# Optimization experiments

Measured on AMD Instinct MI355X. Metric: run time of the kernel, lower is better.

## Reference

```python
import jax, jax.numpy as jnp
import numpy as np
import math

B, SQ, SK = 8, 1024, 1024
DQ = DK = DV = 1024
H = 16
EPS = 1e-5


def _layer_norm(x, g, b):
    mu = jnp.mean(x, axis=-1, keepdims=True)
    var = jnp.mean(jnp.square(x - mu), axis=-1, keepdims=True)
    return (x - mu) * jax.lax.rsqrt(var + EPS) * g + b


def setup_inputs() -> dict:
    key = jax.random.key(0)
    ks = jax.random.split(key, 8)
    s_q = 1.0 / math.sqrt(DQ)
    s_v = 1.0 / math.sqrt(DV)
    return {
        "Q": jax.random.normal(ks[0], (B, SQ, DQ), dtype=jnp.float32),
        "K": jax.random.normal(ks[1], (B, SK, DK), dtype=jnp.float32),
        "Wq": jax.random.normal(ks[2], (DQ, DV), dtype=jnp.float32) * s_q,
        "bq": jnp.zeros((DV,), dtype=jnp.float32),
        "Wk": jax.random.normal(ks[3], (DK, DV), dtype=jnp.float32) * s_q,
        "bk": jnp.zeros((DV,), dtype=jnp.float32),
        "Wv": jax.random.normal(ks[4], (DK, DV), dtype=jnp.float32) * s_q,
        "bv": jnp.zeros((DV,), dtype=jnp.float32),
        "Wo": jax.random.normal(ks[5], (DV, DV), dtype=jnp.float32) * s_v,
        "bo": jnp.zeros((DV,), dtype=jnp.float32),
        "g0": jnp.ones((DV,), dtype=jnp.float32),
        "b0": jnp.zeros((DV,), dtype=jnp.float32),
        "g1": jnp.ones((DV,), dtype=jnp.float32),
        "b1": jnp.zeros((DV,), dtype=jnp.float32),
    }


def reference(Q, K, Wq, bq, Wk, bk, Wv, bv, Wo, bo, g0, b0, g1, b1):
    dh = DV // H
    q = Q @ Wq + bq                      # [B,SQ,DV]
    k = K @ Wk + bk                      # [B,SK,DV]
    v = K @ Wv + bv                      # [B,SK,DV]
    # split/cat over heads == reshape to [B,S,H,dh]
    qh = q.reshape(B, SQ, H, dh)
    kh = k.reshape(B, SK, H, dh)
    vh = v.reshape(B, SK, H, dh)
    # NOTE: original scales by sqrt(dim_V), not sqrt(head_dim)
    scores = jnp.einsum("bqhd,bkhd->bhqk", qh, kh) / math.sqrt(DV)
    A = jax.nn.softmax(scores, axis=-1)  # [B,H,SQ,SK]
    attn = jnp.einsum("bhqk,bkhd->bqhd", A, vh)
    out = q + attn.reshape(B, SQ, DV)    # residual with projected Q
    out = _layer_norm(out, g0, b0)
    out = out + jax.nn.relu(out @ Wo + bo)
    out = _layer_norm(out, g1, b1)
    return out
```

## Files before the change

kernel.cpp:

```cpp
#include <hip/hip_runtime.h>
#include <hip/hip_bf16.h>
#include <stdint.h>

#define NB 8
#define NSQ 1024
#define NSK 1024
#define ND 1024
#define NH 16
#define NDH 64
#define NM (NB * NSQ)
#define LOG2E 1.4426950408889634f

typedef __bf16 bf16;
typedef __bf16 bf16x8 __attribute__((ext_vector_type(8)));
typedef float f32x4 __attribute__((ext_vector_type(4)));
typedef float f32x16 __attribute__((ext_vector_type(16)));
typedef unsigned int uint32;

__device__ __forceinline__ void async_load16(const void* g, void* l) {
  __builtin_amdgcn_global_load_lds(
      (__attribute__((address_space(1))) void*)g,
      (__attribute__((address_space(3))) void*)l, 16, 0, 0);
}

__device__ __forceinline__ void permswap(uint32& x, uint32& y) {
#if __has_builtin(__builtin_amdgcn_permlane32_swap)
  auto r = __builtin_amdgcn_permlane32_swap(x, y, false, false);
  x = r[0]; y = r[1];
#else
  asm volatile("v_permlane32_swap_b32 %0, %1" : "+v"(x), "+v"(y));
#endif
}

__global__ __launch_bounds__(256) void cvt2_f32_bf16(const float* __restrict__ A,
                                                     const float* __restrict__ B,
                                                     bf16* __restrict__ Oa,
                                                     bf16* __restrict__ Ob) {
  const float* in = blockIdx.y ? B : A;
  bf16* out = blockIdx.y ? Ob : Oa;
  int i = blockIdx.x * 256 + threadIdx.x;
  float4 v = *(const float4*)(in + (size_t)i * 4);
  union { uint64_t u; bf16 h[4]; } o;
  o.h[0] = (bf16)v.x; o.h[1] = (bf16)v.y; o.h[2] = (bf16)v.z; o.h[3] = (bf16)v.w;
  *(uint64_t*)(out + (size_t)i * 4) = o.u;
}

__global__ __launch_bounds__(256) void transpose_cvt4(
    const float* __restrict__ W0, const float* __restrict__ W1,
    const float* __restrict__ W2, const float* __restrict__ W3,
    bf16* __restrict__ O0, bf16* __restrict__ O1,
    bf16* __restrict__ O2, bf16* __restrict__ O3) {
  const float* W; bf16* Wt;
  switch (blockIdx.z) {
    case 0: W = W0; Wt = O0; break;
    case 1: W = W1; Wt = O1; break;
    case 2: W = W2; Wt = O2; break;
    default: W = W3; Wt = O3; break;
  }
  __shared__ float t[64][65];
  const int bc = blockIdx.x * 64;
  const int br = blockIdx.y * 64;
  const int tid = threadIdx.x;
  for (int c = tid; c < 1024; c += 256) {
    int r = c >> 4, off = (c & 15) * 4;
    float4 v = *(const float4*)&W[(size_t)(br + r) * 1024 + bc + off];
    t[r][off] = v.x; t[r][off + 1] = v.y; t[r][off + 2] = v.z; t[r][off + 3] = v.w;
  }
  __syncthreads();
  for (int c = tid; c < 512; c += 256) {
    int cc = c >> 3, rr = (c & 7) * 8;
    union { uint4 u; bf16 h[8]; } o;
#pragma unroll
    for (int i = 0; i < 8; ++i) o.h[i] = (bf16)t[rr + i][cc];
    *(uint4*)&Wt[(size_t)(bc + cc) * 1024 + br + rr] = o.u;
  }
}

__global__ __launch_bounds__(256) void transpose_v(const bf16* __restrict__ vsrc,
                                                   bf16* __restrict__ vT) {
  const int st = blockIdx.x * 64;
  const int bh = blockIdx.y;
  const int b = bh >> 4, h = bh & 15;
  __shared__ __align__(16) bf16 t[64][72];
  const int tid = threadIdx.x;
  for (int c = tid; c < 512; c += 256) {
    int s = c >> 3, off = (c & 7) * 8;
    *(uint4*)&t[s][off] =
        *(const uint4*)&vsrc[(size_t)(b * NSK + st + s) * 2048 + 1024 + h * NDH + off];
  }
  __syncthreads();
  for (int c = tid; c < 512; c += 256) {
    int d = c >> 3, s0 = (c & 7) * 8;
    union { uint4 u; bf16 h[8]; } o;
#pragma unroll
    for (int i = 0; i < 8; ++i) o.h[i] = t[s0 + i][d];
    *(uint4*)&vT[((size_t)(bh * NDH + d)) * NSK + st + s0] = o.u;
  }
}

template <int BM, int MODE, int NXC>
__global__ __launch_bounds__(256, 2) void gemm3b(
    const bf16* __restrict__ A, const bf16* __restrict__ Bt,
    const float* __restrict__ bias, const float* __restrict__ bias2,
    bf16* __restrict__ Cb, const bf16* __restrict__ Resb, float scale, int N) {
  constexpr int NT = 32;
  constexpr int AR = BM / 64;
  constexpr int MR = BM / 32;
  __shared__ __align__(16) bf16 Asl[3][BM * 32];
  __shared__ __align__(16) bf16 Bsl[3][128 * 32];

  const int tid = threadIdx.x;
  const int flat = blockIdx.x;
  const int xi = (flat & 7) * 64 + (flat >> 3);
  const int bcol = (xi & (NXC - 1)) * 128;
  const int brow = (xi / NXC) * BM;

  const int w = tid >> 6, lane = tid & 63;
  const int wm = w >> 1, wn = w & 1;
  const int lr = lane & 15, l4 = lane >> 4;
  const int rgrp = l4 * 4;
  const int gph = (l4 ^ ((lr >> 1) & 3)) * 8;

  const int srow = tid >> 2;
  const int gsrc = (tid & 3) ^ ((tid >> 3) & 3);
  const bf16* Ag = A + (size_t)(brow + srow) * 1024 + gsrc * 8;
  const bf16* Bg = Bt + (size_t)(bcol + srow) * 1024 + gsrc * 8;
  const int ldo = srow * 32 + (tid & 3) * 8;

  auto stage = [&](int d, int kt) {
#pragma unroll
    for (int r = 0; r < AR; ++r)
      async_load16(Ag + (size_t)r * (64 * 1024) + kt * 32, &Asl[d][r * 2048 + ldo]);
#pragma unroll
    for (int r = 0; r < 2; ++r)
      async_load16(Bg + (size_t)r * (64 * 1024) + kt * 32, &Bsl[d][r * 2048 + ldo]);
  };
  auto wait_tile = [&]() {
    if constexpr (BM == 256) asm volatile("s_waitcnt vmcnt(6)" ::: "memory");
    else                     asm volatile("s_waitcnt vmcnt(4)" ::: "memory");
  };

  f32x4 acc[MR][4] = {};

  stage(0, 0);
  stage(1, 1);
  wait_tile();
  __builtin_amdgcn_s_barrier();

  int cur = 0, st2 = 2;
  for (int t = 0; t < NT; ++t) {
    bf16x8 af[MR], bfr[4];
#pragma unroll
    for (int i = 0; i < MR; ++i)
      af[i] = *(const bf16x8*)&Asl[cur][(wm * (BM / 2) + i * 16 + lr) * 32 + gph];
#pragma unroll
    for (int n = 0; n < 4; ++n)
      bfr[n] = *(const bf16x8*)&Bsl[cur][(wn * 64 + n * 16 + lr) * 32 + gph];
    if (t + 2 < NT) stage(st2, t + 2);
    __builtin_amdgcn_s_setprio(1);
#pragma unroll
    for (int i = 0; i < MR; ++i)
#pragma unroll
      for (int n = 0; n < 4; ++n)
        acc[i][n] = __builtin_amdgcn_mfma_f32_16x16x32_bf16(af[i], bfr[n], acc[i][n], 0, 0, 0);
    __builtin_amdgcn_s_setprio(0);
    if (t + 2 < NT)      wait_tile();
    else if (t + 1 < NT) asm volatile("s_waitcnt vmcnt(0)" ::: "memory");
    asm volatile("s_waitcnt lgkmcnt(0)" ::: "memory");
    __builtin_amdgcn_s_barrier();
    cur = (cur == 2) ? 0 : cur + 1;
    st2 = (st2 == 2) ? 0 : st2 + 1;
  }

#pragma unroll
  for (int m = 0; m < MR; ++m) {
#pragma unroll
    for (int n = 0; n < 4; ++n) {
      const int col = bcol + wn * 64 + n * 16 + lr;
      float bv, sc;
      if (MODE == 2) {
        const bool isV = (bcol >= 1024);
        bv = isV ? bias2[col - 1024] : bias[col];
        sc = isV ? 1.0f : LOG2E;
      } else {
        bv = bias[col];
        sc = scale;
      }
#pragma unroll
      for (int r = 0; r < 4; ++r) {
        const int row = brow + wm * (BM / 2) + m * 16 + rgrp + r;
        float v = acc[m][n][r] + bv;
        if (MODE == 1) {
          float res = (float)Resb[(size_t)row * N + col];
          Cb[(size_t)row * N + col] = (bf16)(res + (v > 0.f ? v : 0.f));
        } else {
          Cb[(size_t)row * N + col] = (bf16)(v * sc);
        }
      }
    }
  }
}

__global__ __launch_bounds__(512, 4) void attn_kernel(
    const bf16* __restrict__ qb, const bf16* __restrict__ kvb,
    const bf16* __restrict__ vT, bf16* __restrict__ attnout) {
  const int bh = blockIdx.y;
  const int b = bh >> 4, h = bh & 15;
  const int tid = threadIdx.x, w = tid >> 6, lane = tid & 63;
  const int l31 = lane & 31;
  const int l1 = lane >> 5;
  const int q0w = blockIdx.x * 256 + w * 32;

  __shared__ __align__(16) bf16 Kl[2][64 * 64];
  __shared__ __align__(16) bf16 Vl[2][64 * 64];

  const int srow = tid >> 3;
  const int sgran = tid & 7;
  const int gsw = sgran ^ (srow & 7);
  const int ldst = srow * 64 + sgran * 8;
  const int rg = l31 & 7;

  const bf16* kbase = kvb + (size_t)(b * NSK) * 2048 + h * NDH;
  const bf16* vbase = vT + (size_t)(bh * NDH) * NSK;

  bf16x8 qf[4];
#pragma unroll
  for (int kd = 0; kd < 4; ++kd)
    qf[kd] = *(const bf16x8*)&qb[(size_t)(b * NSQ + q0w + l31) * ND +
                                 h * NDH + kd * 16 + l1 * 8];

  f32x16 oacc0 = {}, oacc1 = {}, lacc = {};
  bf16x8 ones;
#pragma unroll
  for (int i = 0; i < 8; ++i) ones[i] = (bf16)1.0f;

  auto stage = [&](int bi, int kt) {
    async_load16(kbase + (size_t)(kt + srow) * 2048 + gsw * 8, &Kl[bi][ldst]);
    async_load16(vbase + (size_t)srow * NSK + kt + gsw * 8, &Vl[bi][ldst]);
  };

  stage(0, 0);

  for (int t = 0; t < 16; ++t) {
    const int bi = t & 1;
    asm volatile("s_waitcnt vmcnt(0)" ::: "memory");
    __syncthreads();
    if (t < 15) stage(bi ^ 1, (t + 1) * 64);

    uint32 W[2][4][2];
#pragma unroll
    for (int n = 0; n < 2; ++n) {
      f32x16 s = {};
      __builtin_amdgcn_s_setprio(1);
#pragma unroll
      for (int kd = 0; kd < 4; ++kd) {
        bf16x8 kf = *(const bf16x8*)&Kl[bi][(n * 32 + l31) * 64 + (((kd * 2 + l1) ^ rg) * 8)];
        s = __builtin_amdgcn_mfma_f32_32x32x16_bf16(kf, qf[kd], s, 0, 0, 0);
      }
      __builtin_amdgcn_s_setprio(0);
#pragma unroll
      for (int r2 = 0; r2 < 4; ++r2)
#pragma unroll
        for (int p = 0; p < 2; ++p) {
          float elo = __builtin_amdgcn_exp2f(s[r2 * 4 + 2 * p]);
          float ehi = __builtin_amdgcn_exp2f(s[r2 * 4 + 2 * p + 1]);
          uint32 wd;
          asm("v_cvt_pk_bf16_f32 %0, %1, %2" : "=v"(wd) : "v"(elo), "v"(ehi));
          W[n][r2][p] = wd;
        }
    }
    __builtin_amdgcn_s_setprio(1);
#pragma unroll
    for (int kc = 0; kc < 4; ++kc) {
      uint32 x0 = W[kc >> 1][(kc & 1) * 2][0], y0 = W[kc >> 1][(kc & 1) * 2 + 1][0];
      uint32 x1 = W[kc >> 1][(kc & 1) * 2][1], y1 = W[kc >> 1][(kc & 1) * 2 + 1][1];
      permswap(x0, y0);
      permswap(x1, y1);
      union { uint32 u[4]; bf16x8 v; } cvt;
      cvt.u[0] = x0; cvt.u[1] = x1; cvt.u[2] = y0; cvt.u[3] = y1;
      bf16x8 pa = cvt.v;
      bf16x8 vf0 = *(const bf16x8*)&Vl[bi][(l31) * 64 + (((kc * 2 + l1) ^ rg) * 8)];
      bf16x8 vf1 = *(const bf16x8*)&Vl[bi][(32 + l31) * 64 + (((kc * 2 + l1) ^ rg) * 8)];
      oacc0 = __builtin_amdgcn_mfma_f32_32x32x16_bf16(pa, vf0, oacc0, 0, 0, 0);
      oacc1 = __builtin_amdgcn_mfma_f32_32x32x16_bf16(pa, vf1, oacc1, 0, 0, 0);
      lacc = __builtin_amdgcn_mfma_f32_32x32x16_bf16(pa, ones, lacc, 0, 0, 0);
    }
    __builtin_amdgcn_s_setprio(0);
  }

  float inv[16];
#pragma unroll
  for (int r = 0; r < 16; ++r) inv[r] = 1.0f / lacc[r];
#pragma unroll
  for (int r = 0; r < 16; ++r) {
    const int row = q0w + (r & 3) + 8 * (r >> 2) + 4 * l1;
    attnout[(size_t)(b * NSQ + row) * ND + h * NDH + l31] = (bf16)(oacc0[r] * inv[r]);
    attnout[(size_t)(b * NSQ + row) * ND + h * NDH + 32 + l31] = (bf16)(oacc1[r] * inv[r]);
  }
}

template <bool RES, bool OUTF>
__global__ __launch_bounds__(256) void ln_kernel(
    const bf16* __restrict__ x, const bf16* __restrict__ rq, float rscale,
    const float* __restrict__ g, const float* __restrict__ be,
    bf16* __restrict__ yb, float* __restrict__ yf) {
  __shared__ float sm[4];
  const int row = blockIdx.x, tid = threadIdx.x;
  const size_t base = (size_t)row * ND + tid * 4;
  union { uint2 u; bf16 h[4]; } xv;
  xv.u = *(const uint2*)(x + base);
  float v0 = (float)xv.h[0], v1 = (float)xv.h[1], v2 = (float)xv.h[2], v3 = (float)xv.h[3];
  if (RES) {
    union { uint2 u; bf16 h[4]; } q;
    q.u = *(const uint2*)(rq + base);
    v0 += rscale * (float)q.h[0]; v1 += rscale * (float)q.h[1];
    v2 += rscale * (float)q.h[2]; v3 += rscale * (float)q.h[3];
  }
  float s = v0 + v1 + v2 + v3;
#pragma unroll
  for (int off = 32; off > 0; off >>= 1) s += __shfl_down(s, off, 64);
  if ((tid & 63) == 0) sm[tid >> 6] = s;
  __syncthreads();
  const float mean = (sm[0] + sm[1] + sm[2] + sm[3]) * (1.0f / ND);
  __syncthreads();
  const float d0 = v0 - mean, d1 = v1 - mean, d2 = v2 - mean, d3 = v3 - mean;
  float sq = d0 * d0 + d1 * d1 + d2 * d2 + d3 * d3;
#pragma unroll
  for (int off = 32; off > 0; off >>= 1) sq += __shfl_down(sq, off, 64);
  if ((tid & 63) == 0) sm[tid >> 6] = sq;
  __syncthreads();
  const float var = (sm[0] + sm[1] + sm[2] + sm[3]) * (1.0f / ND);
  const float rs = rsqrtf(var + 1e-5f);
  float4 gv = *(const float4*)(g + tid * 4);
  float4 bv = *(const float4*)(be + tid * 4);
  const float y0 = d0 * rs * gv.x + bv.x;
  const float y1 = d1 * rs * gv.y + bv.y;
  const float y2 = d2 * rs * gv.z + bv.z;
  const float y3 = d3 * rs * gv.w + bv.w;
  if (OUTF) {
    *(float4*)(yf + base) = make_float4(y0, y1, y2, y3);
  } else {
    union { uint2 u; bf16 h[4]; } o;
    o.h[0] = (bf16)y0; o.h[1] = (bf16)y1; o.h[2] = (bf16)y2; o.h[3] = (bf16)y3;
    *(uint2*)(yb + base) = o.u;
  }
}

extern "C" void kernel_launch(void* const* d_in, const int* in_sizes, int n_in,
                              void* d_out, int out_size, void* d_ws, size_t ws_size,
                              hipStream_t stream) {
  const float* Q  = (const float*)d_in[0];
  const float* K  = (const float*)d_in[1];
  const float* Wq = (const float*)d_in[2];
  const float* bq = (const float*)d_in[3];
  const float* Wk = (const float*)d_in[4];
  const float* bk = (const float*)d_in[5];
  const float* Wv = (const float*)d_in[6];
  const float* bv = (const float*)d_in[7];
  const float* Wo = (const float*)d_in[8];
  const float* bo = (const float*)d_in[9];
  const float* g0 = (const float*)d_in[10];
  const float* b0 = (const float*)d_in[11];
  const float* g1 = (const float*)d_in[12];
  const float* b1 = (const float*)d_in[13];
  float* out = (float*)d_out;

  char* ws = (char*)d_ws;
  const size_t MB = 1024 * 1024;
  bf16* Qb    = (bf16*)(ws + 0);
  bf16* Kb    = (bf16*)(ws + 16 * MB);
  bf16* Wqt   = (bf16*)(ws + 32 * MB);
  bf16* Wkvt  = (bf16*)(ws + 34 * MB);
  bf16* Wot   = (bf16*)(ws + 38 * MB);
  bf16* qb    = (bf16*)(ws + 40 * MB);
  bf16* kvb   = (bf16*)(ws + 56 * MB);
  bf16* vT    = (bf16*)(ws + 88 * MB);
  bf16* attnb = (bf16*)(ws + 104 * MB);
  bf16* h0b   = (bf16*)(ws + 56 * MB);
  bf16* out1b = (bf16*)(ws + 0);

  cvt2_f32_bf16<<<dim3(8192, 2), 256, 0, stream>>>(Q, K, Qb, Kb);
  transpose_cvt4<<<dim3(16, 16, 4), 256, 0, stream>>>(
      Wq, Wk, Wv, Wo, Wqt, Wkvt, Wkvt + 1024 * 1024, Wot);
  gemm3b<256, 2, 16><<<512, 256, 0, stream>>>(Kb, Wkvt, bk, bv, kvb, nullptr, 1.0f, 2048);
  gemm3b<128, 0, 8><<<512, 256, 0, stream>>>(Qb, Wqt, bq, nullptr, qb, nullptr, 0.03125f, 1024);
  transpose_v<<<dim3(16, 128), 256, 0, stream>>>(kvb, vT);
  attn_kernel<<<dim3(4, 128), 512, 0, stream>>>(qb, kvb, vT, attnb);
  ln_kernel<true, false><<<8192, 256, 0, stream>>>(attnb, qb, 32.0f, g0, b0, h0b, nullptr);
  gemm3b<128, 1, 8><<<512, 256, 0, stream>>>(h0b, Wot, bo, nullptr, out1b, h0b, 1.0f, 1024);
  ln_kernel<false, true><<<8192, 256, 0, stream>>>(out1b, nullptr, 0.f, g1, b1, nullptr, out);
}
```

Baseline: 180.3 us.

## Use 2-wave 256x128 GEMM tiles and remap attention grid for L2 locality

Replaces the 4-wave GEMM kernel with a 2-wave version in which each wave computes a 128x128 sub-tile (8x8 MFMA accumulators), raising per-wave register reuse of LDS fragments, and shrinks the Q and Wo projection grids to 256 blocks of 256x128. The attention kernel moves to a flat 1D grid with a swizzled block-to-(batch,head,q-tile) mapping so that concurrently running blocks are spread across XCDs and share K/V in cache. Risks include very high VGPR use (256 accumulator floats per lane), lower occupancy, and fewer blocks than CUs for the 256-block GEMMs.

```diff
diff --git a/kernel.cpp b/kernel.cpp
--- a/kernel.cpp
+++ b/kernel.cpp
@@ -98,25 +98,23 @@
   }
 }
 
-template <int BM, int MODE, int NXC>
-__global__ __launch_bounds__(256, 2) void gemm3b(
+template <int MODE, int NXC>
+__global__ __launch_bounds__(128) void gemmW(
     const bf16* __restrict__ A, const bf16* __restrict__ Bt,
     const float* __restrict__ bias, const float* __restrict__ bias2,
     bf16* __restrict__ Cb, const bf16* __restrict__ Resb, float scale, int N) {
   constexpr int NT = 32;
-  constexpr int AR = BM / 64;
-  constexpr int MR = BM / 32;
-  __shared__ __align__(16) bf16 Asl[3][BM * 32];
+  __shared__ __align__(16) bf16 Asl[3][256 * 32];
   __shared__ __align__(16) bf16 Bsl[3][128 * 32];
 
   const int tid = threadIdx.x;
   const int flat = blockIdx.x;
-  const int xi = (flat & 7) * 64 + (flat >> 3);
+  const int nwg = gridDim.x;
+  const int xi = (flat & 7) * (nwg >> 3) + (flat >> 3);
   const int bcol = (xi & (NXC - 1)) * 128;
-  const int brow = (xi / NXC) * BM;
+  const int brow = (xi / NXC) * 256;
 
   const int w = tid >> 6, lane = tid & 63;
-  const int wm = w >> 1, wn = w & 1;
   const int lr = lane & 15, l4 = lane >> 4;
   const int rgrp = l4 * 4;
   const int gph = (l4 ^ ((lr >> 1) & 3)) * 8;
@@ -129,42 +127,38 @@
 
   auto stage = [&](int d, int kt) {
 #pragma unroll
-    for (int r = 0; r < AR; ++r)
-      async_load16(Ag + (size_t)r * (64 * 1024) + kt * 32, &Asl[d][r * 2048 + ldo]);
-#pragma unroll
-    for (int r = 0; r < 2; ++r)
-      async_load16(Bg + (size_t)r * (64 * 1024) + kt * 32, &Bsl[d][r * 2048 + ldo]);
+    for (int r = 0; r < 8; ++r)
+      async_load16(Ag + (size_t)r * (32 * 1024) + kt * 32, &Asl[d][r * 1024 + ldo]);
+#pragma unroll
+    for (int r = 0; r < 4; ++r)
+      async_load16(Bg + (size_t)r * (32 * 1024) + kt * 32, &Bsl[d][r * 1024 + ldo]);
   };
-  auto wait_tile = [&]() {
-    if constexpr (BM == 256) asm volatile("s_waitcnt vmcnt(6)" ::: "memory");
-    else                     asm volatile("s_waitcnt vmcnt(4)" ::: "memory");
-  };
-
-  f32x4 acc[MR][4] = {};
+
+  f32x4 acc[8][8] = {};
 
   stage(0, 0);
   stage(1, 1);
-  wait_tile();
+  asm volatile("s_waitcnt vmcnt(12)" ::: "memory");
   __builtin_amdgcn_s_barrier();
 
   int cur = 0, st2 = 2;
   for (int t = 0; t < NT; ++t) {
-    bf16x8 af[MR], bfr[4];
-#pragma unroll
-    for (int i = 0; i < MR; ++i)
-      af[i] = *(const bf16x8*)&Asl[cur][(wm * (BM / 2) + i * 16 + lr) * 32 + gph];
-#pragma unroll
-    for (int n = 0; n < 4; ++n)
-      bfr[n] = *(const bf16x8*)&Bsl[cur][(wn * 64 + n * 16 + lr) * 32 + gph];
+    bf16x8 af[8], bfr[8];
+#pragma unroll
+    for (int i = 0; i < 8; ++i)
+      af[i] = *(const bf16x8*)&Asl[cur][(w * 128 + i * 16 + lr) * 32 + gph];
+#pragma unroll
+    for (int n = 0; n < 8; ++n)
+      bfr[n] = *(const bf16x8*)&Bsl[cur][(n * 16 + lr) * 32 + gph];
     if (t + 2 < NT) stage(st2, t + 2);
     __builtin_amdgcn_s_setprio(1);
 #pragma unroll
-    for (int i = 0; i < MR; ++i)
-#pragma unroll
-      for (int n = 0; n < 4; ++n)
+    for (int i = 0; i < 8; ++i)
+#pragma unroll
+      for (int n = 0; n < 8; ++n)
         acc[i][n] = __builtin_amdgcn_mfma_f32_16x16x32_bf16(af[i], bfr[n], acc[i][n], 0, 0, 0);
     __builtin_amdgcn_s_setprio(0);
-    if (t + 2 < NT)      wait_tile();
+    if (t + 2 < NT)      asm volatile("s_waitcnt vmcnt(12)" ::: "memory");
     else if (t + 1 < NT) asm volatile("s_waitcnt vmcnt(0)" ::: "memory");
     asm volatile("s_waitcnt lgkmcnt(0)" ::: "memory");
     __builtin_amdgcn_s_barrier();
@@ -173,10 +167,10 @@
   }
 
 #pragma unroll
-  for (int m = 0; m < MR; ++m) {
-#pragma unroll
-    for (int n = 0; n < 4; ++n) {
-      const int col = bcol + wn * 64 + n * 16 + lr;
+  for (int m = 0; m < 8; ++m) {
+#pragma unroll
+    for (int n = 0; n < 8; ++n) {
+      const int col = bcol + n * 16 + lr;
       float bv, sc;
       if (MODE == 2) {
         const bool isV = (bcol >= 1024);
@@ -188,7 +182,7 @@
       }
 #pragma unroll
       for (int r = 0; r < 4; ++r) {
-        const int row = brow + wm * (BM / 2) + m * 16 + rgrp + r;
+        const int row = brow + w * 128 + m * 16 + rgrp + r;
         float v = acc[m][n][r] + bv;
         if (MODE == 1) {
           float res = (float)Resb[(size_t)row * N + col];
@@ -204,12 +198,14 @@
 __global__ __launch_bounds__(512, 4) void attn_kernel(
     const bf16* __restrict__ qb, const bf16* __restrict__ kvb,
     const bf16* __restrict__ vT, bf16* __restrict__ attnout) {
-  const int bh = blockIdx.y;
+  const int bid = blockIdx.x;
+  const int bh = (bid & 7) + 8 * ((bid >> 3) & 15);
+  const int qi = bid >> 7;
   const int b = bh >> 4, h = bh & 15;
   const int tid = threadIdx.x, w = tid >> 6, lane = tid & 63;
   const int l31 = lane & 31;
   const int l1 = lane >> 5;
-  const int q0w = blockIdx.x * 256 + w * 32;
+  const int q0w = qi * 256 + w * 32;
 
   __shared__ __align__(16) bf16 Kl[2][64 * 64];
   __shared__ __align__(16) bf16 Vl[2][64 * 64];
@@ -382,11 +378,11 @@
   cvt2_f32_bf16<<<dim3(8192, 2), 256, 0, stream>>>(Q, K, Qb, Kb);
   transpose_cvt4<<<dim3(16, 16, 4), 256, 0, stream>>>(
       Wq, Wk, Wv, Wo, Wqt, Wkvt, Wkvt + 1024 * 1024, Wot);
-  gemm3b<256, 2, 16><<<512, 256, 0, stream>>>(Kb, Wkvt, bk, bv, kvb, nullptr, 1.0f, 2048);
-  gemm3b<128, 0, 8><<<512, 256, 0, stream>>>(Qb, Wqt, bq, nullptr, qb, nullptr, 0.03125f, 1024);
+  gemmW<2, 16><<<512, 128, 0, stream>>>(Kb, Wkvt, bk, bv, kvb, nullptr, 1.0f, 2048);
+  gemmW<0, 8><<<256, 128, 0, stream>>>(Qb, Wqt, bq, nullptr, qb, nullptr, 0.03125f, 1024);
   transpose_v<<<dim3(16, 128), 256, 0, stream>>>(kvb, vT);
-  attn_kernel<<<dim3(4, 128), 512, 0, stream>>>(qb, kvb, vT, attnb);
+  attn_kernel<<<512, 512, 0, stream>>>(qb, kvb, vT, attnb);
   ln_kernel<true, false><<<8192, 256, 0, stream>>>(attnb, qb, 32.0f, g0, b0, h0b, nullptr);
-  gemm3b<128, 1, 8><<<512, 256, 0, stream>>>(h0b, Wot, bo, nullptr, out1b, h0b, 1.0f, 1024);
+  gemmW<1, 8><<<256, 128, 0, stream>>>(h0b, Wot, bo, nullptr, out1b, h0b, 1.0f, 1024);
   ln_kernel<false, true><<<8192, 256, 0, stream>>>(out1b, nullptr, 0.f, g1, b1, nullptr, out);
 }
```

Result: slower. 196.8 us (+9.1%).

## Fuse fp32-to-bf16 input conversion into projection GEMM A-tile loads

Applied to the files above, without the earlier changes.

Removes the separate Q/K fp32→bf16 conversion kernel. The K/V and Q projection GEMMs now load fp32 A tiles into registers, convert them, and write them to LDS one stage ahead, while B still uses async global-to-LDS loads. This avoids a 64MB read plus 32MB write pass and one launch. In exchange, the GEMM reads twice the A bytes from fp32, holds more registers, and adds VALU conversion and LDS stores inside the main loop. The wait counts were retuned to match.

```diff
diff --git a/kernel.cpp b/kernel.cpp
--- a/kernel.cpp
+++ b/kernel.cpp
@@ -30,19 +30,6 @@
 #else
   asm volatile("v_permlane32_swap_b32 %0, %1" : "+v"(x), "+v"(y));
 #endif
-}
-
-__global__ __launch_bounds__(256) void cvt2_f32_bf16(const float* __restrict__ A,
-                                                     const float* __restrict__ B,
-                                                     bf16* __restrict__ Oa,
-                                                     bf16* __restrict__ Ob) {
-  const float* in = blockIdx.y ? B : A;
-  bf16* out = blockIdx.y ? Ob : Oa;
-  int i = blockIdx.x * 256 + threadIdx.x;
-  float4 v = *(const float4*)(in + (size_t)i * 4);
-  union { uint64_t u; bf16 h[4]; } o;
-  o.h[0] = (bf16)v.x; o.h[1] = (bf16)v.y; o.h[2] = (bf16)v.z; o.h[3] = (bf16)v.w;
-  *(uint64_t*)(out + (size_t)i * 4) = o.u;
 }
 
 __global__ __launch_bounds__(256) void transpose_cvt4(
@@ -98,9 +85,10 @@
   }
 }
 
-template <int BM, int MODE, int NXC>
+template <int BM, int MODE, int NXC, bool AF32>
 __global__ __launch_bounds__(256, 2) void gemm3b(
-    const bf16* __restrict__ A, const bf16* __restrict__ Bt,
+    const float* __restrict__ Af, const bf16* __restrict__ Ab,
+    const bf16* __restrict__ Bt,
     const float* __restrict__ bias, const float* __restrict__ bias2,
     bf16* __restrict__ Cb, const bf16* __restrict__ Resb, float scale, int N) {
   constexpr int NT = 32;
@@ -123,28 +111,64 @@
 
   const int srow = tid >> 2;
   const int gsrc = (tid & 3) ^ ((tid >> 3) & 3);
-  const bf16* Ag = A + (size_t)(brow + srow) * 1024 + gsrc * 8;
   const bf16* Bg = Bt + (size_t)(bcol + srow) * 1024 + gsrc * 8;
   const int ldo = srow * 32 + (tid & 3) * 8;
 
-  auto stage = [&](int d, int kt) {
-#pragma unroll
-    for (int r = 0; r < AR; ++r)
-      async_load16(Ag + (size_t)r * (64 * 1024) + kt * 32, &Asl[d][r * 2048 + ldo]);
+  auto stageB = [&](int d, int kt) {
 #pragma unroll
     for (int r = 0; r < 2; ++r)
       async_load16(Bg + (size_t)r * (64 * 1024) + kt * 32, &Bsl[d][r * 2048 + ldo]);
   };
-  auto wait_tile = [&]() {
-    if constexpr (BM == 256) asm volatile("s_waitcnt vmcnt(6)" ::: "memory");
-    else                     asm volatile("s_waitcnt vmcnt(4)" ::: "memory");
+  auto stageA_lds = [&](int d, int kt) {
+#pragma unroll
+    for (int r = 0; r < AR; ++r)
+      async_load16(Ab + (size_t)(brow + srow + r * 64) * 1024 + gsrc * 8 + kt * 32,
+                   &Asl[d][r * 2048 + ldo]);
+  };
+
+  float4 areg[AR][2];
+  auto issueA = [&](int kt) {
+    const float* base = Af + (size_t)(brow + srow) * 1024 + gsrc * 8 + kt * 32;
+#pragma unroll
+    for (int r = 0; r < AR; ++r) {
+      areg[r][0] = *(const float4*)(base + (size_t)r * (64 * 1024));
+      areg[r][1] = *(const float4*)(base + (size_t)r * (64 * 1024) + 4);
+    }
+  };
+  auto writeA = [&](int d) {
+#pragma unroll
+    for (int r = 0; r < AR; ++r) {
+      bf16x8 o;
+      o[0] = (bf16)areg[r][0].x; o[1] = (bf16)areg[r][0].y;
+      o[2] = (bf16)areg[r][0].z; o[3] = (bf16)areg[r][0].w;
+      o[4] = (bf16)areg[r][1].x; o[5] = (bf16)areg[r][1].y;
+      o[6] = (bf16)areg[r][1].z; o[7] = (bf16)areg[r][1].w;
+      *(bf16x8*)&Asl[d][r * 2048 + ldo] = o;
+    }
+  };
+  auto wait_vm_steady = [&]() {
+    if constexpr (AF32) {
+      if constexpr (BM == 256) asm volatile("s_waitcnt vmcnt(10)" ::: "memory");
+      else                     asm volatile("s_waitcnt vmcnt(6)" ::: "memory");
+    } else {
+      if constexpr (BM == 256) asm volatile("s_waitcnt vmcnt(6)" ::: "memory");
+      else                     asm volatile("s_waitcnt vmcnt(4)" ::: "memory");
+    }
   };
 
   f32x4 acc[MR][4] = {};
 
-  stage(0, 0);
-  stage(1, 1);
-  wait_tile();
+  if constexpr (AF32) {
+    issueA(0); stageB(0, 0);
+    writeA(0);
+    issueA(1); stageB(1, 1);
+    wait_vm_steady();
+    asm volatile("s_waitcnt lgkmcnt(0)" ::: "memory");
+  } else {
+    stageA_lds(0, 0); stageB(0, 0);
+    stageA_lds(1, 1); stageB(1, 1);
+    wait_vm_steady();
+  }
   __builtin_amdgcn_s_barrier();
 
   int cur = 0, st2 = 2;
@@ -156,7 +180,12 @@
 #pragma unroll
     for (int n = 0; n < 4; ++n)
       bfr[n] = *(const bf16x8*)&Bsl[cur][(wn * 64 + n * 16 + lr) * 32 + gph];
-    if (t + 2 < NT) stage(st2, t + 2);
+    if constexpr (AF32) {
+      if (t + 1 < NT) writeA((cur == 2) ? 0 : cur + 1);
+      if (t + 2 < NT) { issueA(t + 2); stageB(st2, t + 2); }
+    } else {
+      if (t + 2 < NT) { stageA_lds(st2, t + 2); stageB(st2, t + 2); }
+    }
     __builtin_amdgcn_s_setprio(1);
 #pragma unroll
     for (int i = 0; i < MR; ++i)
@@ -164,7 +193,7 @@
       for (int n = 0; n < 4; ++n)
         acc[i][n] = __builtin_amdgcn_mfma_f32_16x16x32_bf16(af[i], bfr[n], acc[i][n], 0, 0, 0);
     __builtin_amdgcn_s_setprio(0);
-    if (t + 2 < NT)      wait_tile();
+    if (t + 2 < NT)      wait_vm_steady();
     else if (t + 1 < NT) asm volatile("s_waitcnt vmcnt(0)" ::: "memory");
     asm volatile("s_waitcnt lgkmcnt(0)" ::: "memory");
     __builtin_amdgcn_s_barrier();
@@ -367,8 +396,6 @@
 
   char* ws = (char*)d_ws;
   const size_t MB = 1024 * 1024;
-  bf16* Qb    = (bf16*)(ws + 0);
-  bf16* Kb    = (bf16*)(ws + 16 * MB);
   bf16* Wqt   = (bf16*)(ws + 32 * MB);
   bf16* Wkvt  = (bf16*)(ws + 34 * MB);
   bf16* Wot   = (bf16*)(ws + 38 * MB);
@@ -379,14 +406,13 @@
   bf16* h0b   = (bf16*)(ws + 56 * MB);
   bf16* out1b = (bf16*)(ws + 0);
 
-  cvt2_f32_bf16<<<dim3(8192, 2), 256, 0, stream>>>(Q, K, Qb, Kb);
   transpose_cvt4<<<dim3(16, 16, 4), 256, 0, stream>>>(
       Wq, Wk, Wv, Wo, Wqt, Wkvt, Wkvt + 1024 * 1024, Wot);
-  gemm3b<256, 2, 16><<<512, 256, 0, stream>>>(Kb, Wkvt, bk, bv, kvb, nullptr, 1.0f, 2048);
-  gemm3b<128, 0, 8><<<512, 256, 0, stream>>>(Qb, Wqt, bq, nullptr, qb, nullptr, 0.03125f, 1024);
+  gemm3b<256, 2, 16, true><<<512, 256, 0, stream>>>(K, nullptr, Wkvt, bk, bv, kvb, nullptr, 1.0f, 2048);
+  gemm3b<128, 0, 8, true><<<512, 256, 0, stream>>>(Q, nullptr, Wqt, bq, nullptr, qb, nullptr, 0.03125f, 1024);
   transpose_v<<<dim3(16, 128), 256, 0, stream>>>(kvb, vT);
   attn_kernel<<<dim3(4, 128), 512, 0, stream>>>(qb, kvb, vT, attnb);
   ln_kernel<true, false><<<8192, 256, 0, stream>>>(attnb, qb, 32.0f, g0, b0, h0b, nullptr);
-  gemm3b<128, 1, 8><<<512, 256, 0, stream>>>(h0b, Wot, bo, nullptr, out1b, h0b, 1.0f, 1024);
+  gemm3b<128, 1, 8, false><<<512, 256, 0, stream>>>(nullptr, h0b, Wot, bo, nullptr, out1b, h0b, 1.0f, 1024);
   ln_kernel<false, true><<<8192, 256, 0, stream>>>(out1b, nullptr, 0.f, g1, b1, nullptr, out);
 }
```

After: 174.6 us. 3.2% less time.
